# Kernel optimization log

Measured on AMD Instinct MI355X. Metric: run time of the kernel, lower is better.

Reference implementation:

```python
import jax, jax.numpy as jnp
import numpy as np

N = 131072
MUL = 32

# e3nn normalization (irrep_normalization='component', path_normalization='element'):
# alpha_path = w3j_norm * sqrt(ir_out.dim / sum_{paths into same i_out} mul1*mul2)
# 0e output: paths (0e,0e)->0e and (1o,1o)->0e -> fan = 2*32*32 = 2048
# 1o output: paths (0e,1o)->1o and (1o,0e)->1o -> fan = 2048
# 1e output: path  (1o,1o)->1e               -> fan = 1024
_A000 = 1.0 / np.sqrt(2048.0)                    # w3j(0,0,0)=1,        sqrt(1/2048)
_A011 = (1.0 / np.sqrt(3.0)) * np.sqrt(3.0 / 2048.0)   # = 1/sqrt(2048)
_A101 = _A011
_A110 = (1.0 / np.sqrt(3.0)) * np.sqrt(1.0 / 2048.0)
_A111 = (1.0 / np.sqrt(6.0)) * np.sqrt(3.0 / 1024.0)   # = 1/sqrt(2048)


def setup_inputs() -> dict:
    key = jax.random.key(0)
    ks = jax.random.split(key, 7)
    return {
        "x1": jax.random.normal(ks[0], (N, 4 * MUL), dtype=jnp.float32),
        "x2": jax.random.normal(ks[1], (N, 4 * MUL), dtype=jnp.float32),
        "w000": jax.random.normal(ks[2], (MUL, MUL, MUL), dtype=jnp.float32),
        "w011": jax.random.normal(ks[3], (MUL, MUL, MUL), dtype=jnp.float32),
        "w101": jax.random.normal(ks[4], (MUL, MUL, MUL), dtype=jnp.float32),
        "w110": jax.random.normal(ks[5], (MUL, MUL, MUL), dtype=jnp.float32),
        "w111": jax.random.normal(ks[6], (MUL, MUL, MUL), dtype=jnp.float32),
    }


def _uvw(a, b, w):
    # scalar-channel path: out_zw = sum_uv a_zu b_zv w_uvw
    return jnp.einsum('zu,zv,uvw->zw', a, b, w, optimize=True)


def _tp(x1, x2, w000, w011, w101, w110, w111):
    n = x1.shape[0]
    x1s = x1[:, :MUL]                       # [z,u]    0e
    x1v = x1[:, MUL:].reshape(n, MUL, 3)    # [z,u,3]  1o
    x2s = x2[:, :MUL]
    x2v = x2[:, MUL:].reshape(n, MUL, 3)

    # (0e,0e)->0e and (1o,1o)->0e  (w3j(1,1,0) = delta_ij/sqrt(3), folded into alpha)
    p000 = _uvw(x1s, x2s, w000)                                  # [z,w]
    p110 = jnp.einsum('zui,zvi,uvw->zw', x1v, x2v, w110, optimize=True)
    out0 = _A000 * p000 + _A110 * p110                           # [z,w]

    # (0e,1o)->1o and (1o,0e)->1o  (w3j(0,1,1) = delta/sqrt(3), folded into alpha)
    p011 = jnp.einsum('zu,zvj,uvw->zwj', x1s, x2v, w011, optimize=True)
    p101 = jnp.einsum('zui,zv,uvw->zwi', x1v, x2s, w101, optimize=True)
    out1 = _A011 * p011 + _A101 * p101                           # [z,w,3]

    # (1o,1o)->1e via levi-civita (w3j(1,1,1) = eps/sqrt(6), folded into alpha)
    # out_zwk = sum_ij eps_ijk * uvw-contraction; expand cross product per component
    comps = []
    for (i, j) in ((1, 2), (2, 0), (0, 1)):
        comps.append(_uvw(x1v[:, :, i], x2v[:, :, j], w111)
                     - _uvw(x1v[:, :, j], x2v[:, :, i], w111))
    out2 = _A111 * jnp.stack(comps, axis=-1)                     # [z,w,3]

    return jnp.concatenate(
        [out0, out1.reshape(n, -1), out2.reshape(n, -1)], axis=-1)  # [z,224]


def reference(x1, x2, w000, w011, w101, w110, w111):
    return _tp(x1, x2, w000, w011, w101, w110, w111)
```

## Files before the change

kernel.cpp:

```cpp
#include <hip/hip_runtime.h>


typedef _Float16 f16;
typedef f16 f16x8 __attribute__((ext_vector_type(8)));
typedef float f32x16 __attribute__((ext_vector_type(16)));

#define MFMA32(a, b, c) __builtin_amdgcn_mfma_f32_32x32x16_f16(a, b, c, 0, 0, 0)

#define SC_COMMON 0.022097086912079608f
#define SC_110    0.012757759118834242f

__global__ void prep_w(const float* __restrict__ w000, const float* __restrict__ w011,
                       const float* __restrict__ w101, const float* __restrict__ w110,
                       const float* __restrict__ w111, f16* __restrict__ wsW)
{
    int flat = blockIdx.x * 256 + threadIdx.x;
    if (flat >= 5 * 32768) return;
    int c    = flat >> 15;
    int r    = flat & 32767;
    int j    = r & 7;
    int lane = (r >> 3) & 63;
    int vh   = (r >> 9) & 1;
    int u    = r >> 10;
    int v = vh * 16 + ((lane >> 5) << 3) + j;
    int w = lane & 31;
    const float* src; float sc;
    switch (c) {
        case 0: src = w000; sc = SC_COMMON; break;
        case 1: src = w110; sc = SC_110;    break;
        case 2: src = w011; sc = SC_COMMON; break;
        case 3: src = w101; sc = SC_COMMON; break;
        default: src = w111; sc = SC_COMMON; break;
    }
    wsW[flat] = (f16)(sc * src[u * 1024 + v * 32 + w]);
}

template <int U0, int MODE, int NA>
__device__ __forceinline__ void do_stage(f32x16 (&acc)[NA],
                                         const f16* __restrict__ ldsW,
                                         const f16x8 (&f1g)[4][4],
                                         const f16x8 (&f2g)[4][2], int lane)
{
#pragma unroll
    for (int ul = 0; ul < 16; ++ul) {
        const int u = U0 + ul;
#pragma unroll
        for (int vh = 0; vh < 2; ++vh) {
            f16x8 b = *(const f16x8*)(ldsW + ul * 1024 + vh * 512 + lane * 8);
            if (MODE == 0) {
                f16x8 a = f1g[0][u >> 3][u & 7] * f2g[0][vh];
                acc[0] = MFMA32(a, b, acc[0]);
            } else if (MODE == 1) {
                f16x8 a = f1g[1][u >> 3][u & 7] * f2g[1][vh];
                a += f1g[2][u >> 3][u & 7] * f2g[2][vh];
                a += f1g[3][u >> 3][u & 7] * f2g[3][vh];
                acc[0] = MFMA32(a, b, acc[0]);
            } else if (MODE == 2) {
#pragma unroll
                for (int j = 0; j < 3; ++j) {
                    f16x8 a = f1g[0][u >> 3][u & 7] * f2g[1 + j][vh];
                    acc[j] = MFMA32(a, b, acc[j]);
                }
            } else if (MODE == 3) {
#pragma unroll
                for (int j = 0; j < 3; ++j) {
                    f16x8 a = f1g[1 + j][u >> 3][u & 7] * f2g[0][vh];
                    acc[j] = MFMA32(a, b, acc[j]);
                }
            } else {
#pragma unroll
                for (int k = 0; k < 3; ++k) {
                    const int P = (k == 0) ? 2 : (k == 1) ? 3 : 1;
                    const int Q = (k == 0) ? 3 : (k == 1) ? 1 : 2;
                    f16x8 a = f1g[P][u >> 3][u & 7] * f2g[Q][vh]
                            - f1g[Q][u >> 3][u & 7] * f2g[P][vh];
                    acc[k] = MFMA32(a, b, acc[k]);
                }
            }
        }
    }
}

__global__ __launch_bounds__(256, 2)
void tp_main(const float* __restrict__ x1, const float* __restrict__ x2,
             const f16* __restrict__ wsW, float* __restrict__ out)
{
    __shared__ __align__(16) f16 ldsW[16384];

    const int tid = threadIdx.x, lane = tid & 63, wv = tid >> 6;
    const int rowBase = blockIdx.x * 128 + wv * 32;
    const int mrow = lane & 31;
    const int half = lane >> 5;
    const int klo = half * 8;
    const float4* x1r4 = (const float4*)(x1 + (size_t)(rowBase + mrow) * 128);
    const float4* x2r4 = (const float4*)(x2 + (size_t)(rowBase + mrow) * 128);

    f16x8 f1g[4][4];
    {
        float b0[32];
#pragma unroll
        for (int g = 0; g < 8; ++g) ((float4*)b0)[g] = x1r4[g];
#pragma unroll
        for (int g = 0; g < 4; ++g)
#pragma unroll
            for (int j = 0; j < 8; ++j) f1g[0][g][j] = (f16)b0[g * 8 + j];
        float b1[96];
#pragma unroll
        for (int g = 0; g < 24; ++g) ((float4*)b1)[g] = x1r4[8 + g];
#pragma unroll
        for (int i = 0; i < 3; ++i)
#pragma unroll
            for (int g = 0; g < 4; ++g)
#pragma unroll
                for (int j = 0; j < 8; ++j)
                    f1g[1 + i][g][j] = (f16)b1[3 * (g * 8 + j) + i];
    }

    f16x8 f2g[4][2];
    {
        float c0[16];
#pragma unroll
        for (int g = 0; g < 2; ++g) ((float4*)c0)[g]     = x2r4[klo / 4 + g];
#pragma unroll
        for (int g = 0; g < 2; ++g) ((float4*)c0)[2 + g] = x2r4[4 + klo / 4 + g];
#pragma unroll
        for (int vh = 0; vh < 2; ++vh)
#pragma unroll
            for (int j = 0; j < 8; ++j) f2g[0][vh][j] = (f16)c0[vh * 8 + j];
        float c1[48];
        const int base1 = (32 + 3 * klo) / 4;
#pragma unroll
        for (int g = 0; g < 6; ++g) ((float4*)c1)[g]     = x2r4[base1 + g];
#pragma unroll
        for (int g = 0; g < 6; ++g) ((float4*)c1)[6 + g] = x2r4[base1 + 12 + g];
#pragma unroll
        for (int i = 0; i < 3; ++i)
#pragma unroll
            for (int vh = 0; vh < 2; ++vh)
#pragma unroll
                for (int j = 0; j < 8; ++j)
                    f2g[1 + i][vh][j] = (f16)c1[vh * 24 + 3 * j + i];
    }

    auto stage = [&](int c, int h) {
        __syncthreads();
        const f16* src = wsW + c * 32768 + h * 16384;
#pragma unroll
        for (int it = 0; it < 8; ++it) {
            int o = (it * 256 + tid) * 8;
            __builtin_amdgcn_global_load_lds(
                (const __attribute__((address_space(1))) void*)(src + o),
                (__attribute__((address_space(3))) void*)(ldsW + o), 16, 0, 0);
        }
        __syncthreads();
    };

    {
        f32x16 acc[1] = {};
        stage(0, 0); do_stage<0, 0>(acc, ldsW, f1g, f2g, lane);
        stage(0, 1); do_stage<16, 0>(acc, ldsW, f1g, f2g, lane);
        stage(1, 0); do_stage<0, 1>(acc, ldsW, f1g, f2g, lane);
        stage(1, 1); do_stage<16, 1>(acc, ldsW, f1g, f2g, lane);
#pragma unroll
        for (int reg = 0; reg < 16; ++reg) {
            int r = (reg & 3) + 8 * (reg >> 2) + 4 * half;
            out[(size_t)(rowBase + r) * 224 + mrow] = acc[0][reg];
        }
    }
    {
        f32x16 acc[3] = {};
        stage(2, 0); do_stage<0, 2>(acc, ldsW, f1g, f2g, lane);
        stage(2, 1); do_stage<16, 2>(acc, ldsW, f1g, f2g, lane);
        stage(3, 0); do_stage<0, 3>(acc, ldsW, f1g, f2g, lane);
        stage(3, 1); do_stage<16, 3>(acc, ldsW, f1g, f2g, lane);
#pragma unroll
        for (int reg = 0; reg < 16; ++reg) {
            int r = (reg & 3) + 8 * (reg >> 2) + 4 * half;
            size_t base = (size_t)(rowBase + r) * 224 + 32 + 3 * mrow;
            out[base + 0] = acc[0][reg];
            out[base + 1] = acc[1][reg];
            out[base + 2] = acc[2][reg];
        }
    }
    {
        f32x16 acc[3] = {};
        stage(4, 0); do_stage<0, 4>(acc, ldsW, f1g, f2g, lane);
        stage(4, 1); do_stage<16, 4>(acc, ldsW, f1g, f2g, lane);
#pragma unroll
        for (int reg = 0; reg < 16; ++reg) {
            int r = (reg & 3) + 8 * (reg >> 2) + 4 * half;
            size_t base = (size_t)(rowBase + r) * 224 + 128 + 3 * mrow;
            out[base + 0] = acc[0][reg];
            out[base + 1] = acc[1][reg];
            out[base + 2] = acc[2][reg];
        }
    }
}

extern "C" void kernel_launch(void* const* d_in, const int* in_sizes, int n_in,
                              void* d_out, int out_size, void* d_ws, size_t ws_size,
                              hipStream_t stream)
{
    const float* x1   = (const float*)d_in[0];
    const float* x2   = (const float*)d_in[1];
    const float* w000 = (const float*)d_in[2];
    const float* w011 = (const float*)d_in[3];
    const float* w101 = (const float*)d_in[4];
    const float* w110 = (const float*)d_in[5];
    const float* w111 = (const float*)d_in[6];
    float* out = (float*)d_out;
    f16* wsW = (f16*)d_ws;

    hipLaunchKernelGGL(prep_w, dim3(640), dim3(256), 0, stream,
                       w000, w011, w101, w110, w111, wsW);

    int n = in_sizes[0] / 128;
    hipLaunchKernelGGL(tp_main, dim3(n / 128), dim3(256), 0, stream,
                       x1, x2, wsW, out);
}
```

Measured before the change: 293.9 us.

## Double-buffer LDS weight stages to overlap global loads with MFMA compute

Splits the LDS weight buffer into two halves and issues the async global-to-LDS load for the next weight slice before computing on the current one. The first slice load is also issued before the x1/x2 register loads and conversions, so those overlap. This hides weight-fetch latency and drops one barrier per stage. In exchange, LDS use per block doubles to 64 KB, which could limit occupancy. Correctness also depends on the barriers ordering the async LDS writes.

```diff
diff --git a/kernel.cpp b/kernel.cpp
--- a/kernel.cpp
+++ b/kernel.cpp
@@ -85,7 +85,7 @@
 void tp_main(const float* __restrict__ x1, const float* __restrict__ x2,
              const f16* __restrict__ wsW, float* __restrict__ out)
 {
-    __shared__ __align__(16) f16 ldsW[16384];
+    __shared__ __align__(16) f16 ldsW[2][16384];
 
     const int tid = threadIdx.x, lane = tid & 63, wv = tid >> 6;
     const int rowBase = blockIdx.x * 128 + wv * 32;
@@ -95,72 +95,77 @@
     const float4* x1r4 = (const float4*)(x1 + (size_t)(rowBase + mrow) * 128);
     const float4* x2r4 = (const float4*)(x2 + (size_t)(rowBase + mrow) * 128);
 
-    f16x8 f1g[4][4];
-    {
-        float b0[32];
-#pragma unroll
-        for (int g = 0; g < 8; ++g) ((float4*)b0)[g] = x1r4[g];
-#pragma unroll
-        for (int g = 0; g < 4; ++g)
-#pragma unroll
-            for (int j = 0; j < 8; ++j) f1g[0][g][j] = (f16)b0[g * 8 + j];
-        float b1[96];
-#pragma unroll
-        for (int g = 0; g < 24; ++g) ((float4*)b1)[g] = x1r4[8 + g];
-#pragma unroll
-        for (int i = 0; i < 3; ++i)
-#pragma unroll
-            for (int g = 0; g < 4; ++g)
-#pragma unroll
-                for (int j = 0; j < 8; ++j)
-                    f1g[1 + i][g][j] = (f16)b1[3 * (g * 8 + j) + i];
-    }
-
-    f16x8 f2g[4][2];
-    {
-        float c0[16];
-#pragma unroll
-        for (int g = 0; g < 2; ++g) ((float4*)c0)[g]     = x2r4[klo / 4 + g];
-#pragma unroll
-        for (int g = 0; g < 2; ++g) ((float4*)c0)[2 + g] = x2r4[4 + klo / 4 + g];
-#pragma unroll
-        for (int vh = 0; vh < 2; ++vh)
-#pragma unroll
-            for (int j = 0; j < 8; ++j) f2g[0][vh][j] = (f16)c0[vh * 8 + j];
-        float c1[48];
-        const int base1 = (32 + 3 * klo) / 4;
-#pragma unroll
-        for (int g = 0; g < 6; ++g) ((float4*)c1)[g]     = x2r4[base1 + g];
-#pragma unroll
-        for (int g = 0; g < 6; ++g) ((float4*)c1)[6 + g] = x2r4[base1 + 12 + g];
-#pragma unroll
-        for (int i = 0; i < 3; ++i)
-#pragma unroll
-            for (int vh = 0; vh < 2; ++vh)
-#pragma unroll
-                for (int j = 0; j < 8; ++j)
-                    f2g[1 + i][vh][j] = (f16)c1[vh * 24 + 3 * j + i];
-    }
-
-    auto stage = [&](int c, int h) {
-        __syncthreads();
-        const f16* src = wsW + c * 32768 + h * 16384;
+    auto issue = [&](int buf, int s) {
+        const f16* src = wsW + s * 16384;
+        f16* dst = &ldsW[buf][0];
 #pragma unroll
         for (int it = 0; it < 8; ++it) {
             int o = (it * 256 + tid) * 8;
             __builtin_amdgcn_global_load_lds(
                 (const __attribute__((address_space(1))) void*)(src + o),
-                (__attribute__((address_space(3))) void*)(ldsW + o), 16, 0, 0);
-        }
-        __syncthreads();
+                (__attribute__((address_space(3))) void*)(dst + o), 16, 0, 0);
+        }
     };
 
+    issue(0, 0);
+
+    f16x8 f1g[4][4];
+    {
+        float b0[32];
+#pragma unroll
+        for (int g = 0; g < 8; ++g) ((float4*)b0)[g] = x1r4[g];
+#pragma unroll
+        for (int g = 0; g < 4; ++g)
+#pragma unroll
+            for (int j = 0; j < 8; ++j) f1g[0][g][j] = (f16)b0[g * 8 + j];
+        float b1[96];
+#pragma unroll
+        for (int g = 0; g < 24; ++g) ((float4*)b1)[g] = x1r4[8 + g];
+#pragma unroll
+        for (int i = 0; i < 3; ++i)
+#pragma unroll
+            for (int g = 0; g < 4; ++g)
+#pragma unroll
+                for (int j = 0; j < 8; ++j)
+                    f1g[1 + i][g][j] = (f16)b1[3 * (g * 8 + j) + i];
+    }
+
+    f16x8 f2g[4][2];
+    {
+        float c0[16];
+#pragma unroll
+        for (int g = 0; g < 2; ++g) ((float4*)c0)[g]     = x2r4[klo / 4 + g];
+#pragma unroll
+        for (int g = 0; g < 2; ++g) ((float4*)c0)[2 + g] = x2r4[4 + klo / 4 + g];
+#pragma unroll
+        for (int vh = 0; vh < 2; ++vh)
+#pragma unroll
+            for (int j = 0; j < 8; ++j) f2g[0][vh][j] = (f16)c0[vh * 8 + j];
+        float c1[48];
+        const int base1 = (32 + 3 * klo) / 4;
+#pragma unroll
+        for (int g = 0; g < 6; ++g) ((float4*)c1)[g]     = x2r4[base1 + g];
+#pragma unroll
+        for (int g = 0; g < 6; ++g) ((float4*)c1)[6 + g] = x2r4[base1 + 12 + g];
+#pragma unroll
+        for (int i = 0; i < 3; ++i)
+#pragma unroll
+            for (int vh = 0; vh < 2; ++vh)
+#pragma unroll
+                for (int j = 0; j < 8; ++j)
+                    f2g[1 + i][vh][j] = (f16)c1[vh * 24 + 3 * j + i];
+    }
+
+    __syncthreads();
+
+
     {
         f32x16 acc[1] = {};
-        stage(0, 0); do_stage<0, 0>(acc, ldsW, f1g, f2g, lane);
-        stage(0, 1); do_stage<16, 0>(acc, ldsW, f1g, f2g, lane);
-        stage(1, 0); do_stage<0, 1>(acc, ldsW, f1g, f2g, lane);
-        stage(1, 1); do_stage<16, 1>(acc, ldsW, f1g, f2g, lane);
+        issue(1, 1); do_stage<0,  0>(acc, ldsW[0], f1g, f2g, lane); __syncthreads();
+        issue(0, 2); do_stage<16, 0>(acc, ldsW[1], f1g, f2g, lane); __syncthreads();
+        issue(1, 3); do_stage<0,  1>(acc, ldsW[0], f1g, f2g, lane); __syncthreads();
+        issue(0, 4); do_stage<16, 1>(acc, ldsW[1], f1g, f2g, lane); __syncthreads();
+        issue(1, 5);
 #pragma unroll
         for (int reg = 0; reg < 16; ++reg) {
             int r = (reg & 3) + 8 * (reg >> 2) + 4 * half;
@@ -169,10 +174,11 @@
     }
     {
         f32x16 acc[3] = {};
-        stage(2, 0); do_stage<0, 2>(acc, ldsW, f1g, f2g, lane);
-        stage(2, 1); do_stage<16, 2>(acc, ldsW, f1g, f2g, lane);
-        stage(3, 0); do_stage<0, 3>(acc, ldsW, f1g, f2g, lane);
-        stage(3, 1); do_stage<16, 3>(acc, ldsW, f1g, f2g, lane);
+         do_stage<0,  2>(acc, ldsW[0], f1g, f2g, lane); __syncthreads();
+        issue(0, 6); do_stage<16, 2>(acc, ldsW[1], f1g, f2g, lane); __syncthreads();
+        issue(1, 7); do_stage<0,  3>(acc, ldsW[0], f1g, f2g, lane); __syncthreads();
+        issue(0, 8); do_stage<16, 3>(acc, ldsW[1], f1g, f2g, lane); __syncthreads();
+        issue(1, 9);
 #pragma unroll
         for (int reg = 0; reg < 16; ++reg) {
             int r = (reg & 3) + 8 * (reg >> 2) + 4 * half;
@@ -184,8 +190,8 @@
     }
     {
         f32x16 acc[3] = {};
-        stage(4, 0); do_stage<0, 4>(acc, ldsW, f1g, f2g, lane);
-        stage(4, 1); do_stage<16, 4>(acc, ldsW, f1g, f2g, lane);
+         do_stage<0,  4>(acc, ldsW[0], f1g, f2g, lane); __syncthreads();
+        do_stage<16, 4>(acc, ldsW[1], f1g, f2g, lane);
 #pragma unroll
         for (int reg = 0; reg < 16; ++reg) {
             int r = (reg & 3) + 8 * (reg >> 2) + 4 * half;
```

After: 280.2 us. 1.05x faster.

## Double-buffer LDS weight stages to overlap global-to-LDS loads with MFMA

Applied to the files above, without the earlier changes.

Splits each weight tile into 8-u chunks held in two alternating LDS buffers. The load of chunk s+1 is issued before chunk s is computed, so the global-to-LDS transfer overlaps with MFMA work instead of stalling behind a barrier. The first chunk's load is also issued before the x1/x2 register loads to hide its latency. In exchange there are more barriers overall, since each chunk is half the old size, and the schedule depends on careful buffer parity and sync ordering.

```diff
diff --git a/kernel.cpp b/kernel.cpp
--- a/kernel.cpp
+++ b/kernel.cpp
@@ -35,45 +35,44 @@
     wsW[flat] = (f16)(sc * src[u * 1024 + v * 32 + w]);
 }
 
-template <int U0, int MODE, int NA>
+template <int Q, int MODE, int NA>
 __device__ __forceinline__ void do_stage(f32x16 (&acc)[NA],
                                          const f16* __restrict__ ldsW,
                                          const f16x8 (&f1g)[4][4],
                                          const f16x8 (&f2g)[4][2], int lane)
 {
 #pragma unroll
-    for (int ul = 0; ul < 16; ++ul) {
-        const int u = U0 + ul;
+    for (int ul = 0; ul < 8; ++ul) {
 #pragma unroll
         for (int vh = 0; vh < 2; ++vh) {
             f16x8 b = *(const f16x8*)(ldsW + ul * 1024 + vh * 512 + lane * 8);
-            if (MODE == 0) {
-                f16x8 a = f1g[0][u >> 3][u & 7] * f2g[0][vh];
+            if constexpr (MODE == 0) {
+                f16x8 a = f1g[0][Q][ul] * f2g[0][vh];
                 acc[0] = MFMA32(a, b, acc[0]);
-            } else if (MODE == 1) {
-                f16x8 a = f1g[1][u >> 3][u & 7] * f2g[1][vh];
-                a += f1g[2][u >> 3][u & 7] * f2g[2][vh];
-                a += f1g[3][u >> 3][u & 7] * f2g[3][vh];
+            } else if constexpr (MODE == 1) {
+                f16x8 a = f1g[1][Q][ul] * f2g[1][vh];
+                a += f1g[2][Q][ul] * f2g[2][vh];
+                a += f1g[3][Q][ul] * f2g[3][vh];
                 acc[0] = MFMA32(a, b, acc[0]);
-            } else if (MODE == 2) {
+            } else if constexpr (MODE == 2) {
 #pragma unroll
                 for (int j = 0; j < 3; ++j) {
-                    f16x8 a = f1g[0][u >> 3][u & 7] * f2g[1 + j][vh];
+                    f16x8 a = f1g[0][Q][ul] * f2g[1 + j][vh];
                     acc[j] = MFMA32(a, b, acc[j]);
                 }
-            } else if (MODE == 3) {
+            } else if constexpr (MODE == 3) {
 #pragma unroll
                 for (int j = 0; j < 3; ++j) {
-                    f16x8 a = f1g[1 + j][u >> 3][u & 7] * f2g[0][vh];
+                    f16x8 a = f1g[1 + j][Q][ul] * f2g[0][vh];
                     acc[j] = MFMA32(a, b, acc[j]);
                 }
             } else {
 #pragma unroll
                 for (int k = 0; k < 3; ++k) {
-                    const int P = (k == 0) ? 2 : (k == 1) ? 3 : 1;
-                    const int Q = (k == 0) ? 3 : (k == 1) ? 1 : 2;
-                    f16x8 a = f1g[P][u >> 3][u & 7] * f2g[Q][vh]
-                            - f1g[Q][u >> 3][u & 7] * f2g[P][vh];
+                    constexpr int PP[3] = {2, 3, 1};
+                    constexpr int QQ[3] = {3, 1, 2};
+                    f16x8 a = f1g[PP[k]][Q][ul] * f2g[QQ[k]][vh]
+                            - f1g[QQ[k]][Q][ul] * f2g[PP[k]][vh];
                     acc[k] = MFMA32(a, b, acc[k]);
                 }
             }
@@ -85,7 +84,7 @@
 void tp_main(const float* __restrict__ x1, const float* __restrict__ x2,
              const f16* __restrict__ wsW, float* __restrict__ out)
 {
-    __shared__ __align__(16) f16 ldsW[16384];
+    __shared__ __align__(16) f16 ldsW[2][8192];
 
     const int tid = threadIdx.x, lane = tid & 63, wv = tid >> 6;
     const int rowBase = blockIdx.x * 128 + wv * 32;
@@ -95,6 +94,20 @@
     const float4* x1r4 = (const float4*)(x1 + (size_t)(rowBase + mrow) * 128);
     const float4* x2r4 = (const float4*)(x2 + (size_t)(rowBase + mrow) * 128);
 
+    auto issue = [&](int s) {
+        const f16* src = wsW + (size_t)s * 8192;
+        f16* dst = &ldsW[s & 1][0];
+#pragma unroll
+        for (int it = 0; it < 4; ++it) {
+            int o = (it * 256 + tid) * 8;
+            __builtin_amdgcn_global_load_lds(
+                (const __attribute__((address_space(1))) void*)(src + o),
+                (__attribute__((address_space(3))) void*)(dst + o), 16, 0, 0);
+        }
+    };
+
+    issue(0);
+
     f16x8 f1g[4][4];
     {
         float b0[32];
@@ -142,25 +155,20 @@
                     f2g[1 + i][vh][j] = (f16)c1[vh * 24 + 3 * j + i];
     }
 
-    auto stage = [&](int c, int h) {
-        __syncthreads();
-        const f16* src = wsW + c * 32768 + h * 16384;
-#pragma unroll
-        for (int it = 0; it < 8; ++it) {
-            int o = (it * 256 + tid) * 8;
-            __builtin_amdgcn_global_load_lds(
-                (const __attribute__((address_space(1))) void*)(src + o),
-                (__attribute__((address_space(3))) void*)(ldsW + o), 16, 0, 0);
-        }
-        __syncthreads();
-    };
+    __syncthreads();
+
 
     {
         f32x16 acc[1] = {};
-        stage(0, 0); do_stage<0, 0>(acc, ldsW, f1g, f2g, lane);
-        stage(0, 1); do_stage<16, 0>(acc, ldsW, f1g, f2g, lane);
-        stage(1, 0); do_stage<0, 1>(acc, ldsW, f1g, f2g, lane);
-        stage(1, 1); do_stage<16, 1>(acc, ldsW, f1g, f2g, lane);
+        issue(1); do_stage<0, 0>(acc, ldsW[0], f1g, f2g, lane); __syncthreads();
+        issue(2); do_stage<1, 0>(acc, ldsW[1], f1g, f2g, lane); __syncthreads();
+        issue(3); do_stage<2, 0>(acc, ldsW[0], f1g, f2g, lane); __syncthreads();
+        issue(4); do_stage<3, 0>(acc, ldsW[1], f1g, f2g, lane); __syncthreads();
+        issue(5); do_stage<0, 1>(acc, ldsW[0], f1g, f2g, lane); __syncthreads();
+        issue(6); do_stage<1, 1>(acc, ldsW[1], f1g, f2g, lane); __syncthreads();
+        issue(7); do_stage<2, 1>(acc, ldsW[0], f1g, f2g, lane); __syncthreads();
+        issue(8); do_stage<3, 1>(acc, ldsW[1], f1g, f2g, lane); __syncthreads();
+        issue(9);
 #pragma unroll
         for (int reg = 0; reg < 16; ++reg) {
             int r = (reg & 3) + 8 * (reg >> 2) + 4 * half;
@@ -169,10 +177,15 @@
     }
     {
         f32x16 acc[3] = {};
-        stage(2, 0); do_stage<0, 2>(acc, ldsW, f1g, f2g, lane);
-        stage(2, 1); do_stage<16, 2>(acc, ldsW, f1g, f2g, lane);
-        stage(3, 0); do_stage<0, 3>(acc, ldsW, f1g, f2g, lane);
-        stage(3, 1); do_stage<16, 3>(acc, ldsW, f1g, f2g, lane);
+         do_stage<0, 2>(acc, ldsW[0], f1g, f2g, lane); __syncthreads();
+        issue(10); do_stage<1, 2>(acc, ldsW[1], f1g, f2g, lane); __syncthreads();
+        issue(11); do_stage<2, 2>(acc, ldsW[0], f1g, f2g, lane); __syncthreads();
+        issue(12); do_stage<3, 2>(acc, ldsW[1], f1g, f2g, lane); __syncthreads();
+        issue(13); do_stage<0, 3>(acc, ldsW[0], f1g, f2g, lane); __syncthreads();
+        issue(14); do_stage<1, 3>(acc, ldsW[1], f1g, f2g, lane); __syncthreads();
+        issue(15); do_stage<2, 3>(acc, ldsW[0], f1g, f2g, lane); __syncthreads();
+        issue(16); do_stage<3, 3>(acc, ldsW[1], f1g, f2g, lane); __syncthreads();
+        issue(17);
 #pragma unroll
         for (int reg = 0; reg < 16; ++reg) {
             int r = (reg & 3) + 8 * (reg >> 2) + 4 * half;
@@ -184,8 +197,10 @@
     }
     {
         f32x16 acc[3] = {};
-        stage(4, 0); do_stage<0, 4>(acc, ldsW, f1g, f2g, lane);
-        stage(4, 1); do_stage<16, 4>(acc, ldsW, f1g, f2g, lane);
+         do_stage<0, 4>(acc, ldsW[0], f1g, f2g, lane); __syncthreads();
+        issue(18); do_stage<1, 4>(acc, ldsW[1], f1g, f2g, lane); __syncthreads();
+        issue(19); do_stage<2, 4>(acc, ldsW[0], f1g, f2g, lane); __syncthreads();
+                   do_stage<3, 4>(acc, ldsW[1], f1g, f2g, lane);
 #pragma unroll
         for (int reg = 0; reg < 16; ++reg) {
             int r = (reg & 3) + 8 * (reg >> 2) + 4 * half;
```

After: 296.5 us. About the same (+0.9%).
